# Kernel tuning notes

Hardware: AMD Instinct MI355X
Metric: run time of the kernel (lower is better)

## Reference

```python
import jax, jax.numpy as jnp
import numpy as np

ORDER = 2


def _masked_row_mean(v, m, safe_cnt, has_any):
    # v already zeroed outside mask; per-row mean over masked entries
    s = jnp.sum(v, axis=1, keepdims=True) / safe_cnt
    return jnp.where(has_any, s, 0.0)


def high_order_residual(x, mask, order=ORDER):
    """Vectorized faithful version of high_order_residual (braq).
    nanmean over masked entries == masked sum / count; sign/scale/shift
    are only meaningful inside the mask, outputs outside the mask are 0.
    """
    m = mask.astype(x.dtype)                       # (oc, ic)
    cnt = jnp.sum(m, axis=1, keepdims=True)        # (oc, 1)
    safe_cnt = jnp.maximum(cnt, 1.0)
    has_any = cnt > 0
    xm = x * m
    sum_order = jnp.zeros_like(x)
    for _ in range(order):
        residual = (xm - sum_order) * m            # masked residual, 0 outside
        mean = _masked_row_mean(residual, m, safe_cnt, has_any)   # (oc,1)
        centered = (residual - mean) * m           # 0 outside mask
        scale = _masked_row_mean(jnp.abs(centered), m, safe_cnt, has_any)
        binary = jnp.sign(centered) * scale + mean
        sum_order = sum_order + binary * m
    return sum_order


def setup_inputs() -> dict:
    key = jax.random.key(0)
    k1, k2 = jax.random.split(key)
    x = jax.random.normal(k1, (11008, 4096), dtype=jnp.float32) * 0.02
    mask = jax.random.randint(k2, (11008, 4096), 0, 2).astype(jnp.bool_)
    return {"x": x, "mask": mask}


def reference(x, mask):
    return high_order_residual(x, mask, ORDER)
```

## Files before the change

### kernel.cpp

```cpp
#include <hip/hip_runtime.h>
#include <stdint.h>

#define IC   4096
#define BLK  256
#define CPL  16

__device__ __forceinline__ double wsum_d(double v) {
    #pragma unroll
    for (int off = 32; off; off >>= 1) v += __shfl_xor(v, off);
    return v;
}
__device__ __forceinline__ int wsum_i(int v) {
    #pragma unroll
    for (int off = 32; off; off >>= 1) v += __shfl_xor(v, off);
    return v;
}

__global__ __launch_bounds__(BLK) void binarize_kernel(
    const float* __restrict__ x,
    const uint8_t* __restrict__ mask,
    float* __restrict__ out)
{
    const int lane = threadIdx.x & 63;
    const int wid  = threadIdx.x >> 6;
    const int row  = blockIdx.x * (BLK / 64) + wid;

    const uint32_t probe = ((const uint32_t*)mask)[lane];
    const bool mask_is_bytes = __any(probe > 1u);

    const float* xr = x + (size_t)row * IC;

    float4 xf[CPL];
    #pragma unroll
    for (int i = 0; i < CPL; ++i)
        xf[i] = ((const float4*)xr)[i * 64 + lane];

    uint64_t bm = 0;
    if (mask_is_bytes) {
        const uint32_t* mr = (const uint32_t*)(mask + (size_t)row * IC);
        #pragma unroll
        for (int i = 0; i < CPL; ++i) {
            const uint32_t w = mr[i * 64 + lane];
            uint64_t b = 0;
            if (w & 0x000000ffu) b |= 1ull;
            if (w & 0x0000ff00u) b |= 2ull;
            if (w & 0x00ff0000u) b |= 4ull;
            if (w & 0xff000000u) b |= 8ull;
            bm |= b << (i * 4);
        }
    } else {
        const int4* mr = (const int4*)mask + (size_t)row * (IC / 4);
        #pragma unroll
        for (int i = 0; i < CPL; ++i) {
            int4 m4 = mr[i * 64 + lane];
            uint64_t b = 0;
            if (m4.x) b |= 1ull;
            if (m4.y) b |= 2ull;
            if (m4.z) b |= 4ull;
            if (m4.w) b |= 8ull;
            bm |= b << (i * 4);
        }
    }

    double s = 0.0;
    #pragma unroll
    for (int i = 0; i < CPL; ++i) {
        const float e[4] = {xf[i].x, xf[i].y, xf[i].z, xf[i].w};
        #pragma unroll
        for (int k = 0; k < 4; ++k)
            if ((bm >> (i * 4 + k)) & 1ull) s += (double)e[k];
    }
    s = wsum_d(s);
    const int cnt = wsum_i(__popcll(bm));

    const double dc    = (double)((cnt > 0) ? cnt : 1);
    const double mean1 = (cnt > 0) ? (s / dc) : 0.0;

    double sa = 0.0;
    int    pn = 0;
    #pragma unroll
    for (int i = 0; i < CPL; ++i) {
        const float e[4] = {xf[i].x, xf[i].y, xf[i].z, xf[i].w};
        #pragma unroll
        for (int k = 0; k < 4; ++k) {
            if ((bm >> (i * 4 + k)) & 1ull) {
                const double ce = (double)e[k] - mean1;
                sa += fabs(ce);
                pn += (ce > 0.0) ? 1 : ((ce < 0.0) ? -1 : 0);
            }
        }
    }
    sa = wsum_d(sa);
    pn = wsum_i(pn);

    const double scale1 = (cnt > 0) ? (sa / dc) : 0.0;
    const double s2    = (s - dc * mean1) - scale1 * (double)pn;
    const double mean2 = (cnt > 0) ? (s2 / dc) : 0.0;

    double sd = 0.0;
    #pragma unroll
    for (int i = 0; i < CPL; ++i) {
        const float e[4] = {xf[i].x, xf[i].y, xf[i].z, xf[i].w};
        #pragma unroll
        for (int k = 0; k < 4; ++k) {
            if ((bm >> (i * 4 + k)) & 1ull) {
                const double xd = (double)e[k];
                const double ce = xd - mean1;
                const double t1 = (ce > 0.0) ? scale1 : ((ce < 0.0) ? -scale1 : 0.0);
                const double b1 = t1 + mean1;
                const double r2 = xd - b1;
                sd += fabs(r2 - mean2);
            }
        }
    }
    sd = wsum_d(sd);
    const double scale2 = (cnt > 0) ? (sd / dc) : 0.0;

    float* orow = out + (size_t)row * IC;
    #pragma unroll
    for (int i = 0; i < CPL; ++i) {
        const float e[4] = {xf[i].x, xf[i].y, xf[i].z, xf[i].w};
        float4 o;
        float* op = &o.x;
        #pragma unroll
        for (int k = 0; k < 4; ++k) {
            if ((bm >> (i * 4 + k)) & 1ull) {
                const double xd = (double)e[k];
                const double ce = xd - mean1;
                const double t1 = (ce > 0.0) ? scale1 : ((ce < 0.0) ? -scale1 : 0.0);
                const double b1 = t1 + mean1;
                const double r2 = xd - b1;
                const double c2 = r2 - mean2;
                const double t2 = (c2 > 0.0) ? scale2 : ((c2 < 0.0) ? -scale2 : 0.0);
                const double b2 = t2 + mean2;
                op[k] = (float)(b1 + b2);
            } else {
                op[k] = 0.0f;
            }
        }
        ((float4*)orow)[i * 64 + lane] = o;
    }
}

extern "C" void kernel_launch(void* const* d_in, const int* in_sizes, int n_in,
                              void* d_out, int out_size, void* d_ws, size_t ws_size,
                              hipStream_t stream) {
    const float*   x    = (const float*)d_in[0];
    const uint8_t* mask = (const uint8_t*)d_in[1];
    float*         out  = (float*)d_out;

    const int rows = in_sizes[0] / IC;
    const int grid = rows / (BLK / 64);
    binarize_kernel<<<grid, BLK, 0, stream>>>(x, mask, out);
}
```

Baseline: 497.9 us.

## Process one row per block with shared-memory reductions and branchless FP64 math

Switches from one wavefront per row (16 float4 per lane) to one 256-thread block per row (4 float4 per thread). Cross-wave reductions now go through shared memory with barriers. Each thread holds fewer registers, which should allow more waves in flight to hide memory latency. Mask packing uses a multiply trick, and the per-element loops become branchless with precomputed A/B constants and split accumulators. The cost is three block barriers per row in exchange for that occupancy and ILP.

After: 403.6 us. 1.23x faster.

```diff
diff --git a/kernel.cpp b/kernel.cpp
--- a/kernel.cpp
+++ b/kernel.cpp
@@ -3,7 +3,7 @@
 
 #define IC   4096
 #define BLK  256
-#define CPL  16
+#define CPT  4
 
 __device__ __forceinline__ double wsum_d(double v) {
     #pragma unroll
@@ -21,124 +21,175 @@
     const uint8_t* __restrict__ mask,
     float* __restrict__ out)
 {
-    const int lane = threadIdx.x & 63;
-    const int wid  = threadIdx.x >> 6;
-    const int row  = blockIdx.x * (BLK / 64) + wid;
+    __shared__ double sm_d[4];
+    __shared__ int    sm_i[4];
+
+    const int tid  = threadIdx.x;
+    const int lane = tid & 63;
+    const int wid  = tid >> 6;
+    const int row  = blockIdx.x;
 
     const uint32_t probe = ((const uint32_t*)mask)[lane];
     const bool mask_is_bytes = __any(probe > 1u);
 
     const float* xr = x + (size_t)row * IC;
 
-    float4 xf[CPL];
-    #pragma unroll
-    for (int i = 0; i < CPL; ++i)
-        xf[i] = ((const float4*)xr)[i * 64 + lane];
-
-    uint64_t bm = 0;
+    float4 xf[CPT];
+    #pragma unroll
+    for (int i = 0; i < CPT; ++i)
+        xf[i] = ((const float4*)xr)[i * BLK + tid];
+
+    uint32_t bm = 0;
     if (mask_is_bytes) {
         const uint32_t* mr = (const uint32_t*)(mask + (size_t)row * IC);
         #pragma unroll
-        for (int i = 0; i < CPL; ++i) {
-            const uint32_t w = mr[i * 64 + lane];
-            uint64_t b = 0;
-            if (w & 0x000000ffu) b |= 1ull;
-            if (w & 0x0000ff00u) b |= 2ull;
-            if (w & 0x00ff0000u) b |= 4ull;
-            if (w & 0xff000000u) b |= 8ull;
-            bm |= b << (i * 4);
+        for (int i = 0; i < CPT; ++i) {
+            const uint32_t w = mr[i * BLK + tid];
+            bm |= (((w * 0x01020408u) >> 24) & 0xFu) << (4 * i);
         }
     } else {
         const int4* mr = (const int4*)mask + (size_t)row * (IC / 4);
         #pragma unroll
-        for (int i = 0; i < CPL; ++i) {
-            int4 m4 = mr[i * 64 + lane];
-            uint64_t b = 0;
-            if (m4.x) b |= 1ull;
-            if (m4.y) b |= 2ull;
-            if (m4.z) b |= 4ull;
-            if (m4.w) b |= 8ull;
-            bm |= b << (i * 4);
-        }
-    }
-
-    double s = 0.0;
-    #pragma unroll
-    for (int i = 0; i < CPL; ++i) {
+        for (int i = 0; i < CPT; ++i) {
+            int4 m4 = mr[i * BLK + tid];
+            uint32_t b = (m4.x ? 1u : 0u) | (m4.y ? 2u : 0u)
+                       | (m4.z ? 4u : 0u) | (m4.w ? 8u : 0u);
+            bm |= b << (4 * i);
+        }
+    }
+
+    double a0 = 0.0, a1 = 0.0, a2 = 0.0, a3 = 0.0;
+    #pragma unroll
+    for (int i = 0; i < CPT; ++i) {
+        a0 += (double)(((bm >> (4*i + 0)) & 1u) ? xf[i].x : 0.0f);
+        a1 += (double)(((bm >> (4*i + 1)) & 1u) ? xf[i].y : 0.0f);
+        a2 += (double)(((bm >> (4*i + 2)) & 1u) ? xf[i].z : 0.0f);
+        a3 += (double)(((bm >> (4*i + 3)) & 1u) ? xf[i].w : 0.0f);
+    }
+    {
+        double sw = wsum_d((a0 + a1) + (a2 + a3));
+        int    cw = wsum_i(__popc(bm));
+        if (lane == 0) { sm_d[wid] = sw; sm_i[wid] = cw; }
+    }
+    __syncthreads();
+    const double s   = (sm_d[0] + sm_d[1]) + (sm_d[2] + sm_d[3]);
+    const int    cnt = (sm_i[0] + sm_i[1]) + (sm_i[2] + sm_i[3]);
+    __syncthreads();
+
+    const bool   has   = (cnt > 0);
+    const double dc    = (double)(has ? cnt : 1);
+    const double mean1 = has ? (s / dc) : 0.0;
+
+    double p0 = 0.0, p1 = 0.0, p2 = 0.0, p3 = 0.0;
+    int q = 0;
+    #pragma unroll
+    for (int i = 0; i < CPT; ++i) {
         const float e[4] = {xf[i].x, xf[i].y, xf[i].z, xf[i].w};
-        #pragma unroll
-        for (int k = 0; k < 4; ++k)
-            if ((bm >> (i * 4 + k)) & 1ull) s += (double)e[k];
-    }
-    s = wsum_d(s);
-    const int cnt = wsum_i(__popcll(bm));
-
-    const double dc    = (double)((cnt > 0) ? cnt : 1);
-    const double mean1 = (cnt > 0) ? (s / dc) : 0.0;
-
-    double sa = 0.0;
-    int    pn = 0;
-    #pragma unroll
-    for (int i = 0; i < CPL; ++i) {
+        {
+            const bool b = (bm >> (4*i + 0)) & 1u;
+            const double ce = (double)e[0] - mean1;
+            p0 += b ? fabs(ce) : 0.0;
+            q  += b ? (int)(ce > 0.0) - (int)(ce < 0.0) : 0;
+        }
+        {
+            const bool b = (bm >> (4*i + 1)) & 1u;
+            const double ce = (double)e[1] - mean1;
+            p1 += b ? fabs(ce) : 0.0;
+            q  += b ? (int)(ce > 0.0) - (int)(ce < 0.0) : 0;
+        }
+        {
+            const bool b = (bm >> (4*i + 2)) & 1u;
+            const double ce = (double)e[2] - mean1;
+            p2 += b ? fabs(ce) : 0.0;
+            q  += b ? (int)(ce > 0.0) - (int)(ce < 0.0) : 0;
+        }
+        {
+            const bool b = (bm >> (4*i + 3)) & 1u;
+            const double ce = (double)e[3] - mean1;
+            p3 += b ? fabs(ce) : 0.0;
+            q  += b ? (int)(ce > 0.0) - (int)(ce < 0.0) : 0;
+        }
+    }
+    {
+        double sw = wsum_d((p0 + p1) + (p2 + p3));
+        int    qw = wsum_i(q);
+        if (lane == 0) { sm_d[wid] = sw; sm_i[wid] = qw; }
+    }
+    __syncthreads();
+    const double sa = (sm_d[0] + sm_d[1]) + (sm_d[2] + sm_d[3]);
+    const int    pn = (sm_i[0] + sm_i[1]) + (sm_i[2] + sm_i[3]);
+    __syncthreads();
+
+    const double scale1 = has ? (sa / dc) : 0.0;
+    const double s2    = (s - dc * mean1) - scale1 * (double)pn;
+    const double mean2 = has ? (s2 / dc) : 0.0;
+
+    const double Ap = scale1 + mean1;
+    const double Am = -scale1 + mean1;
+    const double A0 = mean1;
+
+    double d0 = 0.0, d1 = 0.0, d2 = 0.0, d3 = 0.0;
+    #pragma unroll
+    for (int i = 0; i < CPT; ++i) {
         const float e[4] = {xf[i].x, xf[i].y, xf[i].z, xf[i].w};
-        #pragma unroll
-        for (int k = 0; k < 4; ++k) {
-            if ((bm >> (i * 4 + k)) & 1ull) {
-                const double ce = (double)e[k] - mean1;
-                sa += fabs(ce);
-                pn += (ce > 0.0) ? 1 : ((ce < 0.0) ? -1 : 0);
-            }
-        }
-    }
-    sa = wsum_d(sa);
-    pn = wsum_i(pn);
-
-    const double scale1 = (cnt > 0) ? (sa / dc) : 0.0;
-    const double s2    = (s - dc * mean1) - scale1 * (double)pn;
-    const double mean2 = (cnt > 0) ? (s2 / dc) : 0.0;
-
-    double sd = 0.0;
-    #pragma unroll
-    for (int i = 0; i < CPL; ++i) {
-        const float e[4] = {xf[i].x, xf[i].y, xf[i].z, xf[i].w};
-        #pragma unroll
-        for (int k = 0; k < 4; ++k) {
-            if ((bm >> (i * 4 + k)) & 1ull) {
-                const double xd = (double)e[k];
-                const double ce = xd - mean1;
-                const double t1 = (ce > 0.0) ? scale1 : ((ce < 0.0) ? -scale1 : 0.0);
-                const double b1 = t1 + mean1;
-                const double r2 = xd - b1;
-                sd += fabs(r2 - mean2);
-            }
-        }
-    }
-    sd = wsum_d(sd);
-    const double scale2 = (cnt > 0) ? (sd / dc) : 0.0;
+        {
+            const bool b = (bm >> (4*i + 0)) & 1u;
+            const double xd = (double)e[0];
+            const double A  = (xd > mean1) ? Ap : ((xd < mean1) ? Am : A0);
+            const double c2 = (xd - A) - mean2;
+            d0 += b ? fabs(c2) : 0.0;
+        }
+        {
+            const bool b = (bm >> (4*i + 1)) & 1u;
+            const double xd = (double)e[1];
+            const double A  = (xd > mean1) ? Ap : ((xd < mean1) ? Am : A0);
+            const double c2 = (xd - A) - mean2;
+            d1 += b ? fabs(c2) : 0.0;
+        }
+        {
+            const bool b = (bm >> (4*i + 2)) & 1u;
+            const double xd = (double)e[2];
+            const double A  = (xd > mean1) ? Ap : ((xd < mean1) ? Am : A0);
+            const double c2 = (xd - A) - mean2;
+            d2 += b ? fabs(c2) : 0.0;
+        }
+        {
+            const bool b = (bm >> (4*i + 3)) & 1u;
+            const double xd = (double)e[3];
+            const double A  = (xd > mean1) ? Ap : ((xd < mean1) ? Am : A0);
+            const double c2 = (xd - A) - mean2;
+            d3 += b ? fabs(c2) : 0.0;
+        }
+    }
+    {
+        double sw = wsum_d((d0 + d1) + (d2 + d3));
+        if (lane == 0) sm_d[wid] = sw;
+    }
+    __syncthreads();
+    const double sd = (sm_d[0] + sm_d[1]) + (sm_d[2] + sm_d[3]);
+
+    const double scale2 = has ? (sd / dc) : 0.0;
+    const double Bp = scale2 + mean2;
+    const double Bm = -scale2 + mean2;
+    const double B0 = mean2;
 
     float* orow = out + (size_t)row * IC;
     #pragma unroll
-    for (int i = 0; i < CPL; ++i) {
+    for (int i = 0; i < CPT; ++i) {
         const float e[4] = {xf[i].x, xf[i].y, xf[i].z, xf[i].w};
         float4 o;
         float* op = &o.x;
         #pragma unroll
         for (int k = 0; k < 4; ++k) {
-            if ((bm >> (i * 4 + k)) & 1ull) {
-                const double xd = (double)e[k];
-                const double ce = xd - mean1;
-                const double t1 = (ce > 0.0) ? scale1 : ((ce < 0.0) ? -scale1 : 0.0);
-                const double b1 = t1 + mean1;
-                const double r2 = xd - b1;
-                const double c2 = r2 - mean2;
-                const double t2 = (c2 > 0.0) ? scale2 : ((c2 < 0.0) ? -scale2 : 0.0);
-                const double b2 = t2 + mean2;
-                op[k] = (float)(b1 + b2);
-            } else {
-                op[k] = 0.0f;
-            }
-        }
-        ((float4*)orow)[i * 64 + lane] = o;
+            const bool b = (bm >> (4*i + k)) & 1u;
+            const double xd = (double)e[k];
+            const double A  = (xd > mean1) ? Ap : ((xd < mean1) ? Am : A0);
+            const double c2 = (xd - A) - mean2;
+            const double B  = (c2 > 0.0) ? Bp : ((c2 < 0.0) ? Bm : B0);
+            const float  r  = (float)(A + B);
+            op[k] = b ? r : 0.0f;
+        }
+        ((float4*)orow)[i * BLK + tid] = o;
     }
 }
 
@@ -150,6 +201,5 @@
     float*         out  = (float*)d_out;
 
     const int rows = in_sizes[0] / IC;
-    const int grid = rows / (BLK / 64);
-    binarize_kernel<<<grid, BLK, 0, stream>>>(x, mask, out);
-}
+    binarize_kernel<<<rows, BLK, 0, stream>>>(x, mask, out);
+}
```

## Split each row across a whole block with shared-memory reductions, two rows per block

Applied to the files above, without the earlier changes.

Instead of one wavefront owning a full 4096-element row (64 floats held in registers per lane), each 256-thread block now processes two rows, with every thread holding four float4 per row. Per-row sums are combined across the four waves through shared memory, which needs three __syncthreads barriers. Branches become selects, mask bits are packed with a multiply trick, and the per-element sign-then-add arithmetic is precomputed into A/B constants. The aim is lower register pressure and higher occupancy for this memory-bound kernel, paid for with block-level barriers and shared-memory traffic.

Result: faster. 419.3 us (-15.8%).

```diff
diff --git a/kernel.cpp b/kernel.cpp
--- a/kernel.cpp
+++ b/kernel.cpp
@@ -3,7 +3,8 @@
 
 #define IC   4096
 #define BLK  256
-#define CPL  16
+#define CPT  4
+#define RPB  2
 
 __device__ __forceinline__ double wsum_d(double v) {
     #pragma unroll
@@ -21,124 +22,185 @@
     const uint8_t* __restrict__ mask,
     float* __restrict__ out)
 {
-    const int lane = threadIdx.x & 63;
-    const int wid  = threadIdx.x >> 6;
-    const int row  = blockIdx.x * (BLK / 64) + wid;
+    __shared__ double sm_d[RPB][12];
+    __shared__ int    sm_i[RPB][8];
+
+    const int tid  = threadIdx.x;
+    const int lane = tid & 63;
+    const int wid  = tid >> 6;
+    const int row0 = blockIdx.x * RPB;
 
     const uint32_t probe = ((const uint32_t*)mask)[lane];
     const bool mask_is_bytes = __any(probe > 1u);
 
-    const float* xr = x + (size_t)row * IC;
-
-    float4 xf[CPL];
-    #pragma unroll
-    for (int i = 0; i < CPL; ++i)
-        xf[i] = ((const float4*)xr)[i * 64 + lane];
-
-    uint64_t bm = 0;
+    float4 xq[RPB][CPT];
+    #pragma unroll
+    for (int r = 0; r < RPB; ++r) {
+        const float4* xp = (const float4*)(x + (size_t)(row0 + r) * IC);
+        #pragma unroll
+        for (int i = 0; i < CPT; ++i) xq[r][i] = xp[i * BLK + tid];
+    }
+
+    uint32_t bm[RPB];
     if (mask_is_bytes) {
-        const uint32_t* mr = (const uint32_t*)(mask + (size_t)row * IC);
-        #pragma unroll
-        for (int i = 0; i < CPL; ++i) {
-            const uint32_t w = mr[i * 64 + lane];
-            uint64_t b = 0;
-            if (w & 0x000000ffu) b |= 1ull;
-            if (w & 0x0000ff00u) b |= 2ull;
-            if (w & 0x00ff0000u) b |= 4ull;
-            if (w & 0xff000000u) b |= 8ull;
-            bm |= b << (i * 4);
+        #pragma unroll
+        for (int r = 0; r < RPB; ++r) {
+            const uint32_t* mp = (const uint32_t*)(mask + (size_t)(row0 + r) * IC);
+            uint32_t b = 0;
+            #pragma unroll
+            for (int i = 0; i < CPT; ++i)
+                b |= (((mp[i * BLK + tid] * 0x01020408u) >> 24) & 0xFu) << (4 * i);
+            bm[r] = b;
         }
     } else {
-        const int4* mr = (const int4*)mask + (size_t)row * (IC / 4);
-        #pragma unroll
-        for (int i = 0; i < CPL; ++i) {
-            int4 m4 = mr[i * 64 + lane];
-            uint64_t b = 0;
-            if (m4.x) b |= 1ull;
-            if (m4.y) b |= 2ull;
-            if (m4.z) b |= 4ull;
-            if (m4.w) b |= 8ull;
-            bm |= b << (i * 4);
-        }
-    }
-
-    double s = 0.0;
-    #pragma unroll
-    for (int i = 0; i < CPL; ++i) {
-        const float e[4] = {xf[i].x, xf[i].y, xf[i].z, xf[i].w};
-        #pragma unroll
-        for (int k = 0; k < 4; ++k)
-            if ((bm >> (i * 4 + k)) & 1ull) s += (double)e[k];
-    }
-    s = wsum_d(s);
-    const int cnt = wsum_i(__popcll(bm));
-
-    const double dc    = (double)((cnt > 0) ? cnt : 1);
-    const double mean1 = (cnt > 0) ? (s / dc) : 0.0;
-
-    double sa = 0.0;
-    int    pn = 0;
-    #pragma unroll
-    for (int i = 0; i < CPL; ++i) {
-        const float e[4] = {xf[i].x, xf[i].y, xf[i].z, xf[i].w};
-        #pragma unroll
-        for (int k = 0; k < 4; ++k) {
-            if ((bm >> (i * 4 + k)) & 1ull) {
-                const double ce = (double)e[k] - mean1;
-                sa += fabs(ce);
-                pn += (ce > 0.0) ? 1 : ((ce < 0.0) ? -1 : 0);
-            }
-        }
-    }
-    sa = wsum_d(sa);
-    pn = wsum_i(pn);
-
-    const double scale1 = (cnt > 0) ? (sa / dc) : 0.0;
-    const double s2    = (s - dc * mean1) - scale1 * (double)pn;
-    const double mean2 = (cnt > 0) ? (s2 / dc) : 0.0;
-
-    double sd = 0.0;
-    #pragma unroll
-    for (int i = 0; i < CPL; ++i) {
-        const float e[4] = {xf[i].x, xf[i].y, xf[i].z, xf[i].w};
-        #pragma unroll
-        for (int k = 0; k < 4; ++k) {
-            if ((bm >> (i * 4 + k)) & 1ull) {
+        #pragma unroll
+        for (int r = 0; r < RPB; ++r) {
+            const int4* mp = (const int4*)mask + (size_t)(row0 + r) * (IC / 4);
+            uint32_t b = 0;
+            #pragma unroll
+            for (int i = 0; i < CPT; ++i) {
+                int4 m4 = mp[i * BLK + tid];
+                b |= ((m4.x ? 1u : 0u) | (m4.y ? 2u : 0u)
+                    | (m4.z ? 4u : 0u) | (m4.w ? 8u : 0u)) << (4 * i);
+            }
+            bm[r] = b;
+        }
+    }
+
+    double s[RPB];
+    double dc[RPB], inv[RPB], mean1[RPB];
+    bool   has[RPB];
+    {
+        double a0[RPB], a1[RPB];
+        #pragma unroll
+        for (int r = 0; r < RPB; ++r) { a0[r] = 0.0; a1[r] = 0.0; }
+        #pragma unroll
+        for (int i = 0; i < CPT; ++i) {
+            #pragma unroll
+            for (int r = 0; r < RPB; ++r) {
+                a0[r] += (double)(((bm[r] >> (4*i + 0)) & 1u) ? xq[r][i].x : 0.0f);
+                a1[r] += (double)(((bm[r] >> (4*i + 1)) & 1u) ? xq[r][i].y : 0.0f);
+                a0[r] += (double)(((bm[r] >> (4*i + 2)) & 1u) ? xq[r][i].z : 0.0f);
+                a1[r] += (double)(((bm[r] >> (4*i + 3)) & 1u) ? xq[r][i].w : 0.0f);
+            }
+        }
+        #pragma unroll
+        for (int r = 0; r < RPB; ++r) {
+            double sw = wsum_d(a0[r] + a1[r]);
+            int    cw = wsum_i(__popc(bm[r]));
+            if (lane == 0) { sm_d[r][wid] = sw; sm_i[r][wid] = cw; }
+        }
+    }
+    __syncthreads();
+    #pragma unroll
+    for (int r = 0; r < RPB; ++r) {
+        s[r] = (sm_d[r][0] + sm_d[r][1]) + (sm_d[r][2] + sm_d[r][3]);
+        const int c = (sm_i[r][0] + sm_i[r][1]) + (sm_i[r][2] + sm_i[r][3]);
+        has[r]   = (c > 0);
+        dc[r]    = (double)(has[r] ? c : 1);
+        inv[r]   = 1.0 / dc[r];
+        mean1[r] = has[r] ? s[r] * inv[r] : 0.0;
+    }
+
+    double scale1[RPB], mean2[RPB];
+    double Ap[RPB], Am[RPB];
+    {
+        double p0[RPB], p1[RPB];
+        int q[RPB];
+        #pragma unroll
+        for (int r = 0; r < RPB; ++r) { p0[r] = 0.0; p1[r] = 0.0; q[r] = 0; }
+        #pragma unroll
+        for (int i = 0; i < CPT; ++i) {
+            #pragma unroll
+            for (int r = 0; r < RPB; ++r) {
+                const float e[4] = {xq[r][i].x, xq[r][i].y, xq[r][i].z, xq[r][i].w};
+                #pragma unroll
+                for (int k = 0; k < 4; ++k) {
+                    const bool b = (bm[r] >> (4*i + k)) & 1u;
+                    const double ce = (double)e[k] - mean1[r];
+                    double& acc = (k & 1) ? p1[r] : p0[r];
+                    acc  += b ? fabs(ce) : 0.0;
+                    q[r] += b ? (int)(ce > 0.0) - (int)(ce < 0.0) : 0;
+                }
+            }
+        }
+        #pragma unroll
+        for (int r = 0; r < RPB; ++r) {
+            double sw = wsum_d(p0[r] + p1[r]);
+            int    qw = wsum_i(q[r]);
+            if (lane == 0) { sm_d[r][4 + wid] = sw; sm_i[r][4 + wid] = qw; }
+        }
+    }
+    __syncthreads();
+    #pragma unroll
+    for (int r = 0; r < RPB; ++r) {
+        const double sa = (sm_d[r][4] + sm_d[r][5]) + (sm_d[r][6] + sm_d[r][7]);
+        const int    pn = (sm_i[r][4] + sm_i[r][5]) + (sm_i[r][6] + sm_i[r][7]);
+        scale1[r] = has[r] ? sa * inv[r] : 0.0;
+        const double s2 = (s[r] - dc[r] * mean1[r]) - scale1[r] * (double)pn;
+        mean2[r] = has[r] ? s2 * inv[r] : 0.0;
+        Ap[r] = scale1[r] + mean1[r];
+        Am[r] = -scale1[r] + mean1[r];
+    }
+
+    double Bp[RPB], Bm[RPB];
+    {
+        double d0[RPB], d1[RPB];
+        #pragma unroll
+        for (int r = 0; r < RPB; ++r) { d0[r] = 0.0; d1[r] = 0.0; }
+        #pragma unroll
+        for (int i = 0; i < CPT; ++i) {
+            #pragma unroll
+            for (int r = 0; r < RPB; ++r) {
+                const float e[4] = {xq[r][i].x, xq[r][i].y, xq[r][i].z, xq[r][i].w};
+                #pragma unroll
+                for (int k = 0; k < 4; ++k) {
+                    const bool b = (bm[r] >> (4*i + k)) & 1u;
+                    const double xd = (double)e[k];
+                    const double A  = (xd > mean1[r]) ? Ap[r]
+                                    : ((xd < mean1[r]) ? Am[r] : mean1[r]);
+                    const double c2 = (xd - A) - mean2[r];
+                    double& acc = (k & 1) ? d1[r] : d0[r];
+                    acc += b ? fabs(c2) : 0.0;
+                }
+            }
+        }
+        #pragma unroll
+        for (int r = 0; r < RPB; ++r) {
+            double sw = wsum_d(d0[r] + d1[r]);
+            if (lane == 0) sm_d[r][8 + wid] = sw;
+        }
+    }
+    __syncthreads();
+    #pragma unroll
+    for (int r = 0; r < RPB; ++r) {
+        const double sd = (sm_d[r][8] + sm_d[r][9]) + (sm_d[r][10] + sm_d[r][11]);
+        const double scale2 = has[r] ? sd * inv[r] : 0.0;
+        Bp[r] = scale2 + mean2[r];
+        Bm[r] = -scale2 + mean2[r];
+    }
+
+    #pragma unroll
+    for (int r = 0; r < RPB; ++r) {
+        float* orow = out + (size_t)(row0 + r) * IC;
+        #pragma unroll
+        for (int i = 0; i < CPT; ++i) {
+            const float e[4] = {xq[r][i].x, xq[r][i].y, xq[r][i].z, xq[r][i].w};
+            float4 o;
+            float* op = &o.x;
+            #pragma unroll
+            for (int k = 0; k < 4; ++k) {
+                const bool b = (bm[r] >> (4*i + k)) & 1u;
                 const double xd = (double)e[k];
-                const double ce = xd - mean1;
-                const double t1 = (ce > 0.0) ? scale1 : ((ce < 0.0) ? -scale1 : 0.0);
-                const double b1 = t1 + mean1;
-                const double r2 = xd - b1;
-                sd += fabs(r2 - mean2);
-            }
-        }
-    }
-    sd = wsum_d(sd);
-    const double scale2 = (cnt > 0) ? (sd / dc) : 0.0;
-
-    float* orow = out + (size_t)row * IC;
-    #pragma unroll
-    for (int i = 0; i < CPL; ++i) {
-        const float e[4] = {xf[i].x, xf[i].y, xf[i].z, xf[i].w};
-        float4 o;
-        float* op = &o.x;
-        #pragma unroll
-        for (int k = 0; k < 4; ++k) {
-            if ((bm >> (i * 4 + k)) & 1ull) {
-                const double xd = (double)e[k];
-                const double ce = xd - mean1;
-                const double t1 = (ce > 0.0) ? scale1 : ((ce < 0.0) ? -scale1 : 0.0);
-                const double b1 = t1 + mean1;
-                const double r2 = xd - b1;
-                const double c2 = r2 - mean2;
-                const double t2 = (c2 > 0.0) ? scale2 : ((c2 < 0.0) ? -scale2 : 0.0);
-                const double b2 = t2 + mean2;
-                op[k] = (float)(b1 + b2);
-            } else {
-                op[k] = 0.0f;
-            }
-        }
-        ((float4*)orow)[i * 64 + lane] = o;
+                const double A  = (xd > mean1[r]) ? Ap[r]
+                                : ((xd < mean1[r]) ? Am[r] : mean1[r]);
+                const double c2 = (xd - A) - mean2[r];
+                const double B  = (c2 > 0.0) ? Bp[r]
+                                : ((c2 < 0.0) ? Bm[r] : mean2[r]);
+                op[k] = b ? (float)(A + B) : 0.0f;
+            }
+            ((float4*)orow)[i * BLK + tid] = o;
+        }
     }
 }
 
@@ -150,6 +212,5 @@
     float*         out  = (float*)d_out;
 
     const int rows = in_sizes[0] / IC;
-    const int grid = rows / (BLK / 64);
-    binarize_kernel<<<grid, BLK, 0, stream>>>(x, mask, out);
-}
+    binarize_kernel<<<rows / RPB, BLK, 0, stream>>>(x, mask, out);
+}
```
